# Optimization experiments

Measured on AMD Instinct MI355X. Metric: run time of the kernel, lower is better.

The kernel has to match this reference:

```python
import jax, jax.numpy as jnp
import numpy as np

ROUTING_ITER = 3
EPS = 1e-8


def squash(caps, axis=-1, eps=EPS):
    dot = jnp.sum(caps * caps, axis=axis, keepdims=True)
    scale = dot / (1.0 + dot) / jnp.sqrt(dot + eps)
    return scale * caps


def setup_inputs() -> dict:
    key = jax.random.key(0)
    k1, k2, k3 = jax.random.split(key, 3)
    B, I, O, D_in, D_out = 32, 1024, 64, 16, 32
    x = jax.random.normal(k1, (B, I, D_in), dtype=jnp.float32)
    W = jax.random.normal(k2, (1, I, O, D_out, D_in), dtype=jnp.float32) * 0.05
    b = jax.random.normal(k3, (1, 1, O, D_out), dtype=jnp.float32) * 0.05
    return {"x": x, "W": W, "b": b}


def reference(x, W, b):
    # u_hat[b,i,o,d] = sum_n W[0,i,o,d,n] * x[b,i,n]
    u_hat = jnp.einsum('iodn,bin->biod', W[0], x)  # [B, I, O, D_out]
    u_hat_det = jax.lax.stop_gradient(u_hat)
    B, I, O, _ = u_hat.shape
    b_ij = jnp.zeros((B, I, O, 1), dtype=x.dtype)
    v_j = None
    for it in range(ROUTING_ITER):
        c_ij = jax.nn.softmax(b_ij, axis=2)  # over output capsules
        if it == ROUTING_ITER - 1:
            s_j = jnp.sum(c_ij * u_hat, axis=1, keepdims=True) + b  # [B,1,O,D]
            v_j = squash(s_j, axis=-1)
        else:
            s_j = jnp.sum(c_ij * u_hat_det, axis=1, keepdims=True)
            v_j = squash(s_j, axis=-1)
            a_ij = jnp.sum(u_hat_det * v_j, axis=-1, keepdims=True)  # agreement
            b_ij = b_ij + a_ij
    return jnp.squeeze(v_j)  # [B, O, D_out]
```

## Files before the change

kernel.cpp:

```cpp
#include <hip/hip_runtime.h>
#include <hip/hip_bf16.h>
#include <stdint.h>

#define B_  32
#define I_  1024
#define O_  64
#define D_  32
#define N_  16
#define OD_ 2048

__device__ __forceinline__ uint32_t f2bf1(float f) {
  uint32_t u = __float_as_uint(f);
  return (u + 0x7fffu + ((u >> 16) & 1u)) >> 16;
}
__device__ __forceinline__ uint32_t pack2(float a, float b) {
  return f2bf1(a) | (f2bf1(b) << 16);
}
__device__ __forceinline__ void unpack8(uint4 r, float u[8]) {
  u[0] = __uint_as_float(r.x << 16);
  u[1] = __uint_as_float(r.x & 0xffff0000u);
  u[2] = __uint_as_float(r.y << 16);
  u[3] = __uint_as_float(r.y & 0xffff0000u);
  u[4] = __uint_as_float(r.z << 16);
  u[5] = __uint_as_float(r.z & 0xffff0000u);
  u[6] = __uint_as_float(r.w << 16);
  u[7] = __uint_as_float(r.w & 0xffff0000u);
}

__global__ __launch_bounds__(256) void k_einsum(const float* __restrict__ x,
                                                const float* __restrict__ W,
                                                uint16_t* __restrict__ uhat) {
  const int i = blockIdx.x >> 2;
  const int q = blockIdx.x & 3;
  const int t = threadIdx.x;
  const int od0 = q * 512 + t;
  __shared__ float xs[B_ * N_];
  for (int e = t; e < B_ * N_; e += 256) {
    int bb = e >> 4, n = e & 15;
    xs[e] = x[(size_t)bb * (I_ * N_) + (size_t)i * N_ + n];
  }
  float wA[16], wB[16];
  {
    const float4* Wa = (const float4*)(W + (size_t)i * (OD_ * N_) + (size_t)od0 * N_);
    const float4* Wb = (const float4*)(W + (size_t)i * (OD_ * N_) + (size_t)(od0 + 256) * N_);
    #pragma unroll
    for (int qq = 0; qq < 4; ++qq) {
      float4 fa = Wa[qq];
      wA[qq * 4 + 0] = fa.x; wA[qq * 4 + 1] = fa.y;
      wA[qq * 4 + 2] = fa.z; wA[qq * 4 + 3] = fa.w;
      float4 fb = Wb[qq];
      wB[qq * 4 + 0] = fb.x; wB[qq * 4 + 1] = fb.y;
      wB[qq * 4 + 2] = fb.z; wB[qq * 4 + 3] = fb.w;
    }
  }
  __syncthreads();
  #pragma unroll 2
  for (int bb = 0; bb < B_; ++bb) {
    float4 x0 = ((const float4*)(xs + bb * 16))[0];
    float4 x1 = ((const float4*)(xs + bb * 16))[1];
    float4 x2 = ((const float4*)(xs + bb * 16))[2];
    float4 x3 = ((const float4*)(xs + bb * 16))[3];
    float xv[16] = {x0.x, x0.y, x0.z, x0.w, x1.x, x1.y, x1.z, x1.w,
                    x2.x, x2.y, x2.z, x2.w, x3.x, x3.y, x3.z, x3.w};
    float a0 = 0.f, a1 = 0.f;
    #pragma unroll
    for (int n = 0; n < 16; ++n) {
      a0 = fmaf(wA[n], xv[n], a0);
      a1 = fmaf(wB[n], xv[n], a1);
    }
    const size_t base = ((size_t)bb * I_ + i) * OD_ + od0;
    uhat[base]       = (uint16_t)f2bf1(a0);
    uhat[base + 256] = (uint16_t)f2bf1(a1);
  }
}

__global__ __launch_bounds__(256) void k_sum0(const uint4* __restrict__ uhat,
                                              uint4* __restrict__ part) {
  const int b = blockIdx.x >> 6, chunk = blockIdx.x & 63;
  const int t = threadIdx.x;
  float acc[8] = {0.f, 0.f, 0.f, 0.f, 0.f, 0.f, 0.f, 0.f};
  const size_t ubase = (((size_t)b * I_ + (size_t)chunk * 16) * OD_ + (size_t)t * 8) >> 3;
  #pragma unroll 4
  for (int ii = 0; ii < 16; ++ii) {
    uint4 r = uhat[ubase + (size_t)ii * (OD_ / 8)];
    float u[8]; unpack8(r, u);
    #pragma unroll
    for (int j = 0; j < 8; ++j) acc[j] += u[j];
  }
  part[(((size_t)b * 64 + chunk) * OD_ + (size_t)t * 8) >> 3] =
      make_uint4(pack2(acc[0], acc[1]), pack2(acc[2], acc[3]),
                 pack2(acc[4], acc[5]), pack2(acc[6], acc[7]));
}

__global__ __launch_bounds__(256) void k_squash(const uint16_t* __restrict__ part,
                                                const float* __restrict__ bias,
                                                float* __restrict__ vout,
                                                float scale, int addBias) {
  const int lane = threadIdx.x & 63;
  const int row = blockIdx.x * 4 + (threadIdx.x >> 6);
  const int b = row >> 6, o = row & 63;
  const int d = lane & 31;
  const uint16_t* p = part + (size_t)b * (64 * OD_) + (size_t)o * 32 + d;
  float s = 0.f;
  const int c0 = (lane >> 5) * 32;
  for (int c = c0; c < c0 + 32; ++c)
    s += __uint_as_float(((uint32_t)p[(size_t)c * OD_]) << 16);
  s += __shfl_xor(s, 32);
  s *= scale;
  if (addBias) s += bias[o * 32 + d];
  float dot = s * s;
  #pragma unroll
  for (int off = 1; off <= 16; off <<= 1) dot += __shfl_xor(dot, off);
  float sc = dot / (1.f + dot) / sqrtf(dot + 1e-8f);
  if (lane < 32) vout[(size_t)row * 32 + d] = s * sc;
}

__global__ __launch_bounds__(256, 4) void k_route(const uint4* __restrict__ uhat,
                                                  const float* __restrict__ vprev,
                                                  float* __restrict__ bij,
                                                  uint4* __restrict__ part,
                                                  int secondIter) {
  const int b = blockIdx.x >> 6, chunk = blockIdx.x & 63;
  const int t = threadIdx.x;
  __shared__ float abuf[16 * 64];
  float vreg[8];
  {
    const float4* vp = (const float4*)(vprev + (size_t)b * OD_ + (size_t)t * 8);
    float4 v0 = vp[0], v1 = vp[1];
    vreg[0] = v0.x; vreg[1] = v0.y; vreg[2] = v0.z; vreg[3] = v0.w;
    vreg[4] = v1.x; vreg[5] = v1.y; vreg[6] = v1.z; vreg[7] = v1.w;
  }
  const size_t ubase = (((size_t)b * I_ + (size_t)chunk * 16) * OD_ + (size_t)t * 8) >> 3;
  uint4 u4[16];
  #pragma unroll
  for (int ii = 0; ii < 16; ++ii) {
    u4[ii] = uhat[ubase + (size_t)ii * (OD_ / 8)];
    float u[8]; unpack8(u4[ii], u);
    float p = 0.f;
    #pragma unroll
    for (int j = 0; j < 8; ++j) p = fmaf(u[j], vreg[j], p);
    p += __shfl_xor(p, 1);
    p += __shfl_xor(p, 2);
    if ((t & 3) == 0) abuf[ii * 64 + (t >> 2)] = p;
  }
  __syncthreads();
  {
    const int ii = t >> 4;
    const int g = t & 15;
    const int i = chunk * 16 + ii;
    float bn[4];
    const size_t bidx = ((size_t)b * I_ + i) * 64 + g * 4;
    if (secondIter) {
      float4 b0 = *((const float4*)(bij + bidx));
      bn[0] = b0.x + abuf[ii * 64 + g * 4 + 0];
      bn[1] = b0.y + abuf[ii * 64 + g * 4 + 1];
      bn[2] = b0.z + abuf[ii * 64 + g * 4 + 2];
      bn[3] = b0.w + abuf[ii * 64 + g * 4 + 3];
    } else {
      #pragma unroll
      for (int j = 0; j < 4; ++j) bn[j] = abuf[ii * 64 + g * 4 + j];
      *((float4*)(bij + bidx)) = make_float4(bn[0], bn[1], bn[2], bn[3]);
    }
    float m = fmaxf(fmaxf(bn[0], bn[1]), fmaxf(bn[2], bn[3]));
    m = fmaxf(m, __shfl_xor(m, 1));
    m = fmaxf(m, __shfl_xor(m, 2));
    m = fmaxf(m, __shfl_xor(m, 4));
    m = fmaxf(m, __shfl_xor(m, 8));
    float e[4], sm = 0.f;
    #pragma unroll
    for (int j = 0; j < 4; ++j) { e[j] = __expf(bn[j] - m); sm += e[j]; }
    sm += __shfl_xor(sm, 1);
    sm += __shfl_xor(sm, 2);
    sm += __shfl_xor(sm, 4);
    sm += __shfl_xor(sm, 8);
    float inv = 1.f / sm;
    #pragma unroll
    for (int j = 0; j < 4; ++j) abuf[ii * 64 + g * 4 + j] = e[j] * inv;
  }
  __syncthreads();
  float s_acc[8] = {0.f, 0.f, 0.f, 0.f, 0.f, 0.f, 0.f, 0.f};
  const int oq = t >> 2;
  #pragma unroll
  for (int ii = 0; ii < 16; ++ii) {
    float u[8]; unpack8(u4[ii], u);
    const float c = abuf[ii * 64 + oq];
    #pragma unroll
    for (int j = 0; j < 8; ++j) s_acc[j] = fmaf(c, u[j], s_acc[j]);
  }
  part[(((size_t)b * 64 + chunk) * OD_ + (size_t)t * 8) >> 3] =
      make_uint4(pack2(s_acc[0], s_acc[1]), pack2(s_acc[2], s_acc[3]),
                 pack2(s_acc[4], s_acc[5]), pack2(s_acc[6], s_acc[7]));
}

extern "C" void kernel_launch(void* const* d_in, const int* in_sizes, int n_in,
                              void* d_out, int out_size, void* d_ws, size_t ws_size,
                              hipStream_t stream) {
  const float* x    = (const float*)d_in[0];
  const float* W    = (const float*)d_in[1];
  const float* bias = (const float*)d_in[2];
  float* out = (float*)d_out;

  char* ws = (char*)d_ws;
  uint16_t* uhat1 = (uint16_t*)ws;
  uint4*    uhat4 = (uint4*)ws;
  float* bij  = (float*)(ws + 134217728ull);
  uint4* part = (uint4*)(ws + 134217728ull + 8388608ull);
  uint16_t* part16 = (uint16_t*)part;
  float* vbuf = (float*)(ws + 134217728ull + 16777216ull);

  k_einsum<<<dim3(I_ * 4), dim3(256), 0, stream>>>(x, W, uhat1);
  k_sum0  <<<dim3(2048), dim3(256), 0, stream>>>(uhat4, part);
  k_squash<<<dim3(512),  dim3(256), 0, stream>>>(part16, bias, vbuf, 1.f / 64.f, 0);
  k_route <<<dim3(2048), dim3(256), 0, stream>>>(uhat4, vbuf, bij, part, 0);
  k_squash<<<dim3(512),  dim3(256), 0, stream>>>(part16, bias, vbuf, 1.f, 0);
  k_route <<<dim3(2048), dim3(256), 0, stream>>>(uhat4, vbuf, bij, part, 1);
  k_squash<<<dim3(512),  dim3(256), 0, stream>>>(part16, bias, out, 1.f, 1);
}
```

Measured before the change: 314.2 us.

## Restructure routing kernel to one lane per output capsule with register softmax

The routing kernel now maps each lane to one output capsule and walks 8 input capsules per wave. It reads a full 32-wide u_hat row per lane, computes agreement, the softmax over the 64 lanes by wave shuffles, and the weighted accumulation in registers. A register double-buffered prefetch overlaps loads with compute. Partial sums from the four waves are reduced through swizzled shared memory. Each block covers 32 input capsules instead of 16, so the sum0, squash and partial buffers shrink to 32 chunks. This removes two block barriers and the shared-memory round trips, at the cost of much higher register pressure (32 u values, 32 accumulators, 32 v values and prefetch buffers), which may reduce occupancy.

```diff
diff --git a/kernel.cpp b/kernel.cpp
--- a/kernel.cpp
+++ b/kernel.cpp
@@ -16,7 +16,7 @@
 __device__ __forceinline__ uint32_t pack2(float a, float b) {
   return f2bf1(a) | (f2bf1(b) << 16);
 }
-__device__ __forceinline__ void unpack8(uint4 r, float u[8]) {
+__device__ __forceinline__ void unpack8(uint4 r, float* u) {
   u[0] = __uint_as_float(r.x << 16);
   u[1] = __uint_as_float(r.x & 0xffff0000u);
   u[2] = __uint_as_float(r.y << 16);
@@ -76,18 +76,18 @@
 
 __global__ __launch_bounds__(256) void k_sum0(const uint4* __restrict__ uhat,
                                               uint4* __restrict__ part) {
-  const int b = blockIdx.x >> 6, chunk = blockIdx.x & 63;
+  const int b = blockIdx.x >> 5, chunk = blockIdx.x & 31;
   const int t = threadIdx.x;
   float acc[8] = {0.f, 0.f, 0.f, 0.f, 0.f, 0.f, 0.f, 0.f};
-  const size_t ubase = (((size_t)b * I_ + (size_t)chunk * 16) * OD_ + (size_t)t * 8) >> 3;
-  #pragma unroll 4
-  for (int ii = 0; ii < 16; ++ii) {
+  const size_t ubase = (((size_t)b * I_ + (size_t)chunk * 32) * OD_ + (size_t)t * 8) >> 3;
+  #pragma unroll 8
+  for (int ii = 0; ii < 32; ++ii) {
     uint4 r = uhat[ubase + (size_t)ii * (OD_ / 8)];
     float u[8]; unpack8(r, u);
     #pragma unroll
     for (int j = 0; j < 8; ++j) acc[j] += u[j];
   }
-  part[(((size_t)b * 64 + chunk) * OD_ + (size_t)t * 8) >> 3] =
+  part[(((size_t)b * 32 + chunk) * OD_ + (size_t)t * 8) >> 3] =
       make_uint4(pack2(acc[0], acc[1]), pack2(acc[2], acc[3]),
                  pack2(acc[4], acc[5]), pack2(acc[6], acc[7]));
 }
@@ -100,10 +100,10 @@
   const int row = blockIdx.x * 4 + (threadIdx.x >> 6);
   const int b = row >> 6, o = row & 63;
   const int d = lane & 31;
-  const uint16_t* p = part + (size_t)b * (64 * OD_) + (size_t)o * 32 + d;
+  const uint16_t* p = part + (size_t)b * (32 * OD_) + (size_t)o * 32 + d;
   float s = 0.f;
-  const int c0 = (lane >> 5) * 32;
-  for (int c = c0; c < c0 + 32; ++c)
+  const int c0 = (lane >> 5) * 16;
+  for (int c = c0; c < c0 + 16; ++c)
     s += __uint_as_float(((uint32_t)p[(size_t)c * OD_]) << 16);
   s += __shfl_xor(s, 32);
   s *= scale;
@@ -120,76 +120,70 @@
                                                   float* __restrict__ bij,
                                                   uint4* __restrict__ part,
                                                   int secondIter) {
-  const int b = blockIdx.x >> 6, chunk = blockIdx.x & 63;
+  const int b = blockIdx.x >> 5, chunk = blockIdx.x & 31;
   const int t = threadIdx.x;
-  __shared__ float abuf[16 * 64];
-  float vreg[8];
+  const int w = t >> 6, lane = t & 63;
+  __shared__ float red[4][64][32];
+  float vreg[32];
   {
-    const float4* vp = (const float4*)(vprev + (size_t)b * OD_ + (size_t)t * 8);
-    float4 v0 = vp[0], v1 = vp[1];
-    vreg[0] = v0.x; vreg[1] = v0.y; vreg[2] = v0.z; vreg[3] = v0.w;
-    vreg[4] = v1.x; vreg[5] = v1.y; vreg[6] = v1.z; vreg[7] = v1.w;
-  }
-  const size_t ubase = (((size_t)b * I_ + (size_t)chunk * 16) * OD_ + (size_t)t * 8) >> 3;
-  uint4 u4[16];
-  #pragma unroll
-  for (int ii = 0; ii < 16; ++ii) {
-    u4[ii] = uhat[ubase + (size_t)ii * (OD_ / 8)];
-    float u[8]; unpack8(u4[ii], u);
-    float p = 0.f;
-    #pragma unroll
-    for (int j = 0; j < 8; ++j) p = fmaf(u[j], vreg[j], p);
-    p += __shfl_xor(p, 1);
-    p += __shfl_xor(p, 2);
-    if ((t & 3) == 0) abuf[ii * 64 + (t >> 2)] = p;
-  }
+    const float4* vp = (const float4*)(vprev + ((size_t)b * 64 + lane) * 32);
+    #pragma unroll
+    for (int q = 0; q < 8; ++q) {
+      float4 f = vp[q];
+      vreg[q * 4 + 0] = f.x; vreg[q * 4 + 1] = f.y;
+      vreg[q * 4 + 2] = f.z; vreg[q * 4 + 3] = f.w;
+    }
+  }
+  float s_acc[32];
+  #pragma unroll
+  for (int d = 0; d < 32; ++d) s_acc[d] = 0.f;
+  const int i0 = chunk * 32 + w * 8;
+  const uint4* ub = uhat + ((size_t)b * I_ + i0) * 256 + (size_t)lane * 4;
+  uint4 c0 = ub[0], c1 = ub[1], c2 = ub[2], c3 = ub[3];
+  #pragma unroll
+  for (int r = 0; r < 8; ++r) {
+    uint4 n0, n1, n2, n3;
+    if (r < 7) {
+      const uint4* un = ub + (size_t)(r + 1) * 256;
+      n0 = un[0]; n1 = un[1]; n2 = un[2]; n3 = un[3];
+    }
+    float u[32];
+    unpack8(c0, u + 0); unpack8(c1, u + 8); unpack8(c2, u + 16); unpack8(c3, u + 24);
+    float a = 0.f;
+    #pragma unroll
+    for (int d = 0; d < 32; ++d) a = fmaf(u[d], vreg[d], a);
+    const int i = i0 + r;
+    const size_t bidx = ((size_t)b * I_ + i) * 64 + lane;
+    float bn = a;
+    if (secondIter) bn += bij[bidx];
+    else            bij[bidx] = bn;
+    float m = bn;
+    #pragma unroll
+    for (int off = 1; off <= 32; off <<= 1) m = fmaxf(m, __shfl_xor(m, off));
+    float e = __expf(bn - m);
+    float sm = e;
+    #pragma unroll
+    for (int off = 1; off <= 32; off <<= 1) sm += __shfl_xor(sm, off);
+    const float c = e / sm;
+    #pragma unroll
+    for (int d = 0; d < 32; ++d) s_acc[d] = fmaf(c, u[d], s_acc[d]);
+    c0 = n0; c1 = n1; c2 = n2; c3 = n3;
+  }
+  #pragma unroll
+  for (int d = 0; d < 32; ++d) red[w][lane][(d + lane) & 31] = s_acc[d];
   __syncthreads();
   {
-    const int ii = t >> 4;
-    const int g = t & 15;
-    const int i = chunk * 16 + ii;
-    float bn[4];
-    const size_t bidx = ((size_t)b * I_ + i) * 64 + g * 4;
-    if (secondIter) {
-      float4 b0 = *((const float4*)(bij + bidx));
-      bn[0] = b0.x + abuf[ii * 64 + g * 4 + 0];
-      bn[1] = b0.y + abuf[ii * 64 + g * 4 + 1];
-      bn[2] = b0.z + abuf[ii * 64 + g * 4 + 2];
-      bn[3] = b0.w + abuf[ii * 64 + g * 4 + 3];
-    } else {
-      #pragma unroll
-      for (int j = 0; j < 4; ++j) bn[j] = abuf[ii * 64 + g * 4 + j];
-      *((float4*)(bij + bidx)) = make_float4(bn[0], bn[1], bn[2], bn[3]);
-    }
-    float m = fmaxf(fmaxf(bn[0], bn[1]), fmaxf(bn[2], bn[3]));
-    m = fmaxf(m, __shfl_xor(m, 1));
-    m = fmaxf(m, __shfl_xor(m, 2));
-    m = fmaxf(m, __shfl_xor(m, 4));
-    m = fmaxf(m, __shfl_xor(m, 8));
-    float e[4], sm = 0.f;
-    #pragma unroll
-    for (int j = 0; j < 4; ++j) { e[j] = __expf(bn[j] - m); sm += e[j]; }
-    sm += __shfl_xor(sm, 1);
-    sm += __shfl_xor(sm, 2);
-    sm += __shfl_xor(sm, 4);
-    sm += __shfl_xor(sm, 8);
-    float inv = 1.f / sm;
-    #pragma unroll
-    for (int j = 0; j < 4; ++j) abuf[ii * 64 + g * 4 + j] = e[j] * inv;
-  }
-  __syncthreads();
-  float s_acc[8] = {0.f, 0.f, 0.f, 0.f, 0.f, 0.f, 0.f, 0.f};
-  const int oq = t >> 2;
-  #pragma unroll
-  for (int ii = 0; ii < 16; ++ii) {
-    float u[8]; unpack8(u4[ii], u);
-    const float c = abuf[ii * 64 + oq];
-    #pragma unroll
-    for (int j = 0; j < 8; ++j) s_acc[j] = fmaf(c, u[j], s_acc[j]);
-  }
-  part[(((size_t)b * 64 + chunk) * OD_ + (size_t)t * 8) >> 3] =
-      make_uint4(pack2(s_acc[0], s_acc[1]), pack2(s_acc[2], s_acc[3]),
-                 pack2(s_acc[4], s_acc[5]), pack2(s_acc[6], s_acc[7]));
+    const int o = t >> 2, db = (t & 3) * 8;
+    float sum[8];
+    #pragma unroll
+    for (int j = 0; j < 8; ++j) {
+      const int sw = (db + j + o) & 31;
+      sum[j] = red[0][o][sw] + red[1][o][sw] + red[2][o][sw] + red[3][o][sw];
+    }
+    part[(((size_t)b * 32 + chunk) * OD_ + (size_t)t * 8) >> 3] =
+        make_uint4(pack2(sum[0], sum[1]), pack2(sum[2], sum[3]),
+                   pack2(sum[4], sum[5]), pack2(sum[6], sum[7]));
+  }
 }
 
 extern "C" void kernel_launch(void* const* d_in, const int* in_sizes, int n_in,
@@ -206,13 +200,13 @@
   float* bij  = (float*)(ws + 134217728ull);
   uint4* part = (uint4*)(ws + 134217728ull + 8388608ull);
   uint16_t* part16 = (uint16_t*)part;
-  float* vbuf = (float*)(ws + 134217728ull + 16777216ull);
+  float* vbuf = (float*)(ws + 134217728ull + 8388608ull + 4194304ull);
 
   k_einsum<<<dim3(I_ * 4), dim3(256), 0, stream>>>(x, W, uhat1);
-  k_sum0  <<<dim3(2048), dim3(256), 0, stream>>>(uhat4, part);
+  k_sum0  <<<dim3(1024), dim3(256), 0, stream>>>(uhat4, part);
   k_squash<<<dim3(512),  dim3(256), 0, stream>>>(part16, bias, vbuf, 1.f / 64.f, 0);
-  k_route <<<dim3(2048), dim3(256), 0, stream>>>(uhat4, vbuf, bij, part, 0);
+  k_route <<<dim3(1024), dim3(256), 0, stream>>>(uhat4, vbuf, bij, part, 0);
   k_squash<<<dim3(512),  dim3(256), 0, stream>>>(part16, bias, vbuf, 1.f, 0);
-  k_route <<<dim3(2048), dim3(256), 0, stream>>>(uhat4, vbuf, bij, part, 1);
+  k_route <<<dim3(1024), dim3(256), 0, stream>>>(uhat4, vbuf, bij, part, 1);
   k_squash<<<dim3(512),  dim3(256), 0, stream>>>(part16, bias, out, 1.f, 1);
 }
```

New measurement: 520.8 us. 1.66x slower.
